# Kernel tuning notes

Hardware: AMD Instinct MI355X
Metric: run time of the kernel (lower is better)

The kernel has to match this reference:

```python
import jax, jax.numpy as jnp
import numpy as np


def _gcn_layer(feat, src, dst, W, b, n, act):
    # DGL GraphConv, norm='both': D_out^{-1/2} gather-sum D_in^{-1/2}, then XW+b
    e = src.shape[0]
    ones = jnp.ones((e,), dtype=feat.dtype)
    deg_out = jnp.clip(jax.ops.segment_sum(ones, src, num_segments=n), 1.0)
    deg_in = jnp.clip(jax.ops.segment_sum(ones, dst, num_segments=n), 1.0)
    h = feat * jax.lax.rsqrt(deg_out)[:, None]          # [n, d]
    agg = jax.ops.segment_sum(h[src], dst, num_segments=n)  # scatter-add over edges
    h = agg * jax.lax.rsqrt(deg_in)[:, None]
    h = h @ W + b
    if act:
        h = jax.nn.relu(h)
    return h


def setup_inputs() -> dict:
    key = jax.random.key(0)
    ks = jax.random.split(key, 12)
    n0, n1, n2 = 20000, 10000, 5000
    e0, e1, e2 = 640000, 320000, 160000
    in_dim, hid, ncls = 256, 128, 40
    s = 0.02
    return {
        "features": jax.random.normal(ks[0], (n0, in_dim), jnp.float32),
        "src0": jax.random.randint(ks[1], (e0,), 0, n0),
        "dst0": jax.random.randint(ks[2], (e0,), 0, n0),
        "src1": jax.random.randint(ks[3], (e1,), 0, n1),
        "dst1": jax.random.randint(ks[4], (e1,), 0, n1),
        "src2": jax.random.randint(ks[5], (e2,), 0, n2),
        "dst2": jax.random.randint(ks[6], (e2,), 0, n2),
        "P1": jax.random.normal(ks[7], (n0, n1), jnp.float32) * s,
        "P2": jax.random.normal(ks[8], (n1, n2), jnp.float32) * s,
        "W0": jax.random.normal(ks[9], (in_dim, hid), jnp.float32) * s,
        "b0": jnp.zeros((hid,), jnp.float32),
        "W1": jax.random.normal(ks[10], (hid, hid), jnp.float32) * s,
        "b1": jnp.zeros((hid,), jnp.float32),
        "W2": jax.random.normal(ks[11], (hid, ncls), jnp.float32) * s,
        "b2": jnp.zeros((ncls,), jnp.float32),
    }


def reference(features, src0, dst0, src1, dst1, src2, dst2, P1, P2,
              W0, b0, W1, b1, W2, b2):
    n0, n1, n2 = P1.shape[0], P1.shape[1], P2.shape[1]
    # layer 0 on finest graph (dropout is identity in eval mode)
    h = _gcn_layer(features, src0, dst0, W0, b0, n0, act=True)
    h = P1.T @ h                                  # project to level 1: [n1, hid]
    h = _gcn_layer(h, src1, dst1, W1, b1, n1, act=True)
    h = P2.T @ h                                  # project to level 2: [n2, hid]
    emb = h                                       # input to final layer
    h = _gcn_layer(h, src2, dst2, W2, b2, n2, act=False)
    return (h, emb)
```

## Files before the change

kernel.cpp:

```cpp
#include <hip/hip_runtime.h>
#include <stdint.h>

typedef __attribute__((ext_vector_type(8))) short s8v;
typedef __attribute__((ext_vector_type(4))) float f4v;

__device__ __forceinline__ unsigned short f2bf(float x){
  union { float f; uint32_t u; } v; v.f = x;
  uint32_t r = v.u + 0x7FFFu + ((v.u >> 16) & 1u);
  return (unsigned short)(r >> 16);
}
__device__ __forceinline__ float bf2f(unsigned short u){
  union { uint32_t u; float f; } v; v.u = ((uint32_t)u) << 16;
  return v.f;
}

__global__ __launch_bounds__(256) void k_cvt_feat(const float* __restrict__ in,
                                                  unsigned short* __restrict__ out, int n4){
  int i = blockIdx.x*256 + threadIdx.x;
  if (i >= n4) return;
  f4v v = ((const f4v*)in)[i];
  uint2 p;
  p.x = f2bf(v.x) | ((uint32_t)f2bf(v.y) << 16);
  p.y = f2bf(v.z) | ((uint32_t)f2bf(v.w) << 16);
  ((uint2*)out)[i] = p;
}

__global__ __launch_bounds__(256) void k_cvt_w(const float* __restrict__ W0, const float* __restrict__ W1,
                                               const float* __restrict__ W2,
                                               unsigned short* Wt0, unsigned short* Wt1, unsigned short* Wt2){
  int id = blockIdx.x*256 + threadIdx.x;
  if (id < 128*256){ int n = id >> 8, k = id & 255;
    Wt0[n*256 + (k ^ ((n&7)<<3))] = f2bf(W0[(size_t)k*128 + n]); return; }
  id -= 128*256;
  if (id < 128*128){ int n = id >> 7, k = id & 127;
    Wt1[n*128 + (k ^ ((n&7)<<3))] = f2bf(W1[(size_t)k*128 + n]); return; }
  id -= 128*128;
  if (id < 48*128){ int n = id >> 7, k = id & 127;
    Wt2[n*128 + (k ^ ((n&7)<<3))] = (n < 40) ? f2bf(W2[(size_t)k*40 + n]) : (unsigned short)0; return; }
}

__global__ __launch_bounds__(256) void k_count(
    const int* __restrict__ s0, const int* __restrict__ d0, int e0,
    const int* __restrict__ s1, const int* __restrict__ d1, int e1,
    const int* __restrict__ s2, const int* __restrict__ d2, int e2,
    int* ci0, int* co0, int* ci1, int* co1, int* ci2, int* co2,
    int* p0, int* p1, int* p2){
  int id = blockIdx.x*256 + threadIdx.x;
  if (id < e0){ p0[id] = atomicAdd(&ci0[d0[id]], 1); atomicAdd(&co0[s0[id]], 1); return; }
  id -= e0;
  if (id < e1){ p1[id] = atomicAdd(&ci1[d1[id]], 1); atomicAdd(&co1[s1[id]], 1); return; }
  id -= e1;
  if (id < e2){ p2[id] = atomicAdd(&ci2[d2[id]], 1); atomicAdd(&co2[s2[id]], 1); return; }
}

__global__ __launch_bounds__(1024) void k_scan3(const int* c0, int n0, int* o0,
                                                const int* c1, int n1, int* o1,
                                                const int* c2, int n2, int* o2){
  const int* c; int n; int* o;
  if (blockIdx.x == 0){ c = c0; n = n0; o = o0; }
  else if (blockIdx.x == 1){ c = c1; n = n1; o = o1; }
  else { c = c2; n = n2; o = o2; }
  __shared__ int part[1024];
  int t = threadIdx.x;
  int chunk = (n + 1023) / 1024;
  int beg = t*chunk, end = min(beg + chunk, n);
  int s = 0;
  for (int i = beg; i < end; i++) s += c[i];
  part[t] = s; __syncthreads();
  for (int d = 1; d < 1024; d <<= 1){
    int add = (t >= d) ? part[t-d] : 0;
    __syncthreads();
    part[t] += add;
    __syncthreads();
  }
  int prefix = (t > 0) ? part[t-1] : 0;
  for (int i = beg; i < end; i++){ o[i] = prefix; prefix += c[i]; }
  if (t == 1023) o[n] = part[1023];
}

__global__ __launch_bounds__(256) void k_place(
    const int* __restrict__ s0, const int* __restrict__ d0, int e0,
    const int* __restrict__ s1, const int* __restrict__ d1, int e1,
    const int* __restrict__ s2, const int* __restrict__ d2, int e2,
    const int* o0, const int* o1, const int* o2,
    const int* p0, const int* p1, const int* p2,
    int* r0, int* r1, int* r2){
  int id = blockIdx.x*256 + threadIdx.x;
  if (id < e0){ r0[o0[d0[id]] + p0[id]] = s0[id]; return; }
  id -= e0;
  if (id < e1){ r1[o1[d1[id]] + p1[id]] = s1[id]; return; }
  id -= e1;
  if (id < e2){ r2[o2[d2[id]] + p2[id]] = s2[id]; return; }
}

__global__ __launch_bounds__(256) void k_rsq(const int* ci0, const int* co0, int n0,
                                             const int* ci1, const int* co1, int n1,
                                             const int* ci2, const int* co2, int n2,
                                             float* ri0, float* ro0, float* ri1, float* ro1,
                                             float* ri2, float* ro2){
  int id = blockIdx.x*256 + threadIdx.x;
  if (id < n0){ ri0[id] = rsqrtf((float)max(ci0[id],1)); ro0[id] = rsqrtf((float)max(co0[id],1)); return; }
  id -= n0;
  if (id < n1){ ri1[id] = rsqrtf((float)max(ci1[id],1)); ro1[id] = rsqrtf((float)max(co1[id],1)); return; }
  id -= n1;
  if (id < n2){ ri2[id] = rsqrtf((float)max(ci2[id],1)); ro2[id] = rsqrtf((float)max(co2[id],1)); return; }
}

template<int D>
__global__ __launch_bounds__(256) void k_agg(const unsigned short* __restrict__ table,
                                             const int* __restrict__ srt, const int* __restrict__ off,
                                             const float* __restrict__ rsq_out, const float* __restrict__ rsq_in,
                                             unsigned short* __restrict__ outb, int n){
  constexpr int VW = D / 64;
  int wid = threadIdx.x >> 6, lane = threadIdx.x & 63;
  int node = blockIdx.x*4 + wid;
  if (node >= n) return;
  int eb = off[node], ee = off[node+1];
  float acc[VW];
  #pragma unroll
  for (int i = 0; i < VW; i++) acc[i] = 0.f;
  int c0 = lane * VW;
  int e = eb;
  int sNext = (e < ee) ? srt[e] : 0;
  while (e < ee){
    int s = sNext;
    e++;
    sNext = (e < ee) ? srt[e] : 0;
    float w = rsq_out[s];
    const unsigned short* row = table + (size_t)s*D + c0;
    if constexpr (VW == 4){
      ushort4 v = *(const ushort4*)row;
      acc[0] += w * bf2f(v.x); acc[1] += w * bf2f(v.y);
      acc[2] += w * bf2f(v.z); acc[3] += w * bf2f(v.w);
    } else {
      ushort2 v = *(const ushort2*)row;
      acc[0] += w * bf2f(v.x); acc[1] += w * bf2f(v.y);
    }
  }
  float ri = rsq_in[node];
  if constexpr (VW == 4){
    uint2 p;
    p.x = f2bf(acc[0]*ri) | ((uint32_t)f2bf(acc[1]*ri) << 16);
    p.y = f2bf(acc[2]*ri) | ((uint32_t)f2bf(acc[3]*ri) << 16);
    *(uint2*)(outb + (size_t)node*D + c0) = p;
  } else {
    uint32_t p = f2bf(acc[0]*ri) | ((uint32_t)f2bf(acc[1]*ri) << 16);
    *(uint32_t*)(outb + (size_t)node*D + c0) = p;
  }
}

template<int K, int NT, bool RELU>
__global__ __launch_bounds__(256) void k_gemm_nn(const unsigned short* __restrict__ A,
                                                 const unsigned short* __restrict__ Wt,
                                                 const float* __restrict__ bias,
                                                 unsigned short* __restrict__ outT,
                                                 float* __restrict__ outF,
                                                 int M, int ldOut, int Nv){
  __shared__ __align__(16) unsigned short lW[NT*16*K];
  for (int i = threadIdx.x; i < NT*16*K/8; i += 256)
    ((uint4*)lW)[i] = ((const uint4*)Wt)[i];
  __syncthreads();
  int lane = threadIdx.x & 63, w = threadIdx.x >> 6;
  int mb = blockIdx.x*64 + w*16;
  int row = mb + (lane & 15);
  int kg = lane >> 4;
  f4v acc[NT];
  #pragma unroll
  for (int nt = 0; nt < NT; nt++) acc[nt] = (f4v){0.f,0.f,0.f,0.f};
  for (int k0 = 0; k0 < K; k0 += 32){
    s8v a = {0,0,0,0,0,0,0,0};
    if (row < M) a = *(const s8v*)(A + (size_t)row*K + k0 + kg*8);
    #pragma unroll
    for (int nt = 0; nt < NT; nt++){
      int n = nt*16 + (lane & 15);
      s8v b = *(const s8v*)(lW + n*K + ((k0 + kg*8) ^ ((n&7)<<3)));
      acc[nt] = __builtin_amdgcn_mfma_f32_16x16x32_bf16(a, b, acc[nt], 0, 0, 0);
    }
  }
  int m4 = mb + kg*4;
  #pragma unroll
  for (int nt = 0; nt < NT; nt++){
    int n = nt*16 + (lane & 15);
    float bv = (n < Nv) ? bias[n] : 0.f;
    float v0 = acc[nt][0] + bv, v1 = acc[nt][1] + bv, v2 = acc[nt][2] + bv, v3 = acc[nt][3] + bv;
    if (RELU){ v0 = fmaxf(v0,0.f); v1 = fmaxf(v1,0.f); v2 = fmaxf(v2,0.f); v3 = fmaxf(v3,0.f); }
    if (outT){
      if (m4 >= M){ v0 = v1 = v2 = v3 = 0.f; }
      uint2 p;
      p.x = f2bf(v0) | ((uint32_t)f2bf(v1) << 16);
      p.y = f2bf(v2) | ((uint32_t)f2bf(v3) << 16);
      *(uint2*)(outT + (size_t)n*ldOut + (m4 ^ ((n&7)<<3))) = p;
    } else {
      float vv[4] = {v0, v1, v2, v3};
      #pragma unroll
      for (int r = 0; r < 4; r++){
        int m = m4 + r;
        if (m < M && n < Nv) outF[(size_t)m*Nv + n] = vv[r];
      }
    }
  }
}

__global__ __launch_bounds__(256) void k_tn(const float* __restrict__ P, int ldP, int M, int K,
                                            const unsigned short* __restrict__ Bsw, int ldB,
                                            float* __restrict__ part, int Mp,
                                            int KPtiles, int chunkTiles){
  __shared__ __align__(16) unsigned short lA[64*64];
  __shared__ __align__(16) unsigned short lB[128*64];
  int mb = blockIdx.x*64;
  int s  = blockIdx.y;
  int tbeg = s * chunkTiles;
  int tend = min(tbeg + chunkTiles, KPtiles);
  int tid = threadIdx.x, lane = tid & 63, w = tid >> 6;
  int wmBase = (w >> 1)*32, wnBase = (w & 1)*64;
  f4v acc[2][4];
  #pragma unroll
  for (int mt = 0; mt < 2; mt++)
    #pragma unroll
    for (int nt = 0; nt < 4; nt++) acc[mt][nt] = (f4v){0.f,0.f,0.f,0.f};

  for (int t = tbeg; t < tend; t++){
    int k0 = t*64;
    {
      int m2 = (tid & 31)*2;
      int kk = (tid >> 5)*2;
      int gm = mb + m2;
      #pragma unroll
      for (int p = 0; p < 4; p++){
        int kr = kk + p*16;
        int gk = k0 + kr;
        float2 r0 = {0.f,0.f}, r1 = {0.f,0.f};
        bool mok = (gm < M);
        if (mok && gk     < K) r0 = *(const float2*)(P + (size_t)gk*ldP + gm);
        if (mok && gk + 1 < K) r1 = *(const float2*)(P + (size_t)(gk+1)*ldP + gm);
        uint32_t w0 = f2bf(r0.x) | ((uint32_t)f2bf(r1.x) << 16);
        uint32_t w1 = f2bf(r0.y) | ((uint32_t)f2bf(r1.y) << 16);
        *(uint32_t*)(lA + m2*64     + (kr ^ ((m2&7)<<3)))     = w0;
        *(uint32_t*)(lA + (m2+1)*64 + (kr ^ (((m2+1)&7)<<3))) = w1;
      }
    }
    {
      int r  = tid >> 3;
      int cb = (tid & 7)*8;
      #pragma unroll
      for (int p = 0; p < 4; p++){
        int n = p*32 + r;
        uint4 v = *(const uint4*)(Bsw + (size_t)n*ldB + k0 + cb);
        *(uint4*)(lB + n*64 + cb) = v;
      }
    }
    __syncthreads();
    #pragma unroll
    for (int ks = 0; ks < 2; ks++){
      int kbase = ks*32 + (lane >> 4)*8;
      s8v a[2];
      #pragma unroll
      for (int mt = 0; mt < 2; mt++){
        int m = wmBase + mt*16 + (lane & 15);
        a[mt] = *(const s8v*)(lA + m*64 + (kbase ^ ((m&7)<<3)));
      }
      #pragma unroll
      for (int nt = 0; nt < 4; nt++){
        int n = wnBase + nt*16 + (lane & 15);
        s8v b = *(const s8v*)(lB + n*64 + (kbase ^ ((n&7)<<3)));
        #pragma unroll
        for (int mt = 0; mt < 2; mt++)
          acc[mt][nt] = __builtin_amdgcn_mfma_f32_16x16x32_bf16(a[mt], b, acc[mt][nt], 0, 0, 0);
      }
    }
    __syncthreads();
  }
  float* dst = part + (size_t)s*Mp*128;
  #pragma unroll
  for (int mt = 0; mt < 2; mt++){
    int m4 = mb + wmBase + mt*16 + (lane >> 4)*4;
    #pragma unroll
    for (int nt = 0; nt < 4; nt++){
      int n = wnBase + nt*16 + (lane & 15);
      #pragma unroll
      for (int r = 0; r < 4; r++)
        dst[(size_t)(m4 + r)*128 + n] = acc[mt][nt][r];
    }
  }
}

__global__ __launch_bounds__(256) void k_reduce(const float* __restrict__ part, int Mp, int S, int M,
                                                unsigned short* __restrict__ gb, float* __restrict__ embOut){
  int i = blockIdx.x*256 + threadIdx.x;
  int total = Mp*32;
  if (i >= total) return;
  f4v sum = (f4v){0.f,0.f,0.f,0.f};
  for (int p = 0; p < S; p++)
    sum += ((const f4v*)(part + (size_t)p*Mp*128))[i];
  int m = (i*4) >> 7;
  if (m < M){
    uint2 pk;
    pk.x = f2bf(sum.x) | ((uint32_t)f2bf(sum.y) << 16);
    pk.y = f2bf(sum.z) | ((uint32_t)f2bf(sum.w) << 16);
    ((uint2*)gb)[i] = pk;
    if (embOut) ((f4v*)embOut)[i] = sum;
  }
}

extern "C" void kernel_launch(void* const* d_in, const int* in_sizes, int n_in,
                              void* d_out, int out_size, void* d_ws, size_t ws_size,
                              hipStream_t stream){
  const float* features = (const float*)d_in[0];
  const int* src0 = (const int*)d_in[1];
  const int* dst0 = (const int*)d_in[2];
  const int* src1 = (const int*)d_in[3];
  const int* dst1 = (const int*)d_in[4];
  const int* src2 = (const int*)d_in[5];
  const int* dst2 = (const int*)d_in[6];
  const float* P1 = (const float*)d_in[7];
  const float* P2 = (const float*)d_in[8];
  const float* W0 = (const float*)d_in[9];
  const float* b0 = (const float*)d_in[10];
  const float* W1 = (const float*)d_in[11];
  const float* b1 = (const float*)d_in[12];
  const float* W2 = (const float*)d_in[13];
  const float* b2 = (const float*)d_in[14];
  float* out = (float*)d_out;

  const int IND = 256, HID = 128, NC = 40;
  const int n0 = in_sizes[0] / IND;
  const int e0 = in_sizes[1], e1 = in_sizes[3], e2 = in_sizes[5];
  const int n1 = (int)((size_t)in_sizes[7] / n0);
  const int n2 = (int)((size_t)in_sizes[8] / n1);

  const int g0   = (n0 + 63)/64;
  const int g1   = (n1 + 63)/64;
  const int g2   = (n2 + 63)/64;
  const int ld1  = g0*64;
  const int ld2  = g1*64;
  const int Mp1  = g1*64;
  const int Mp2  = g2*64;
  const int S1 = 6, S2 = 8;
  const int KPt1 = g0;
  const int KPt2 = g1;
  const int cT1 = (KPt1 + S1 - 1)/S1;
  const int cT2 = (KPt2 + S2 - 1)/S2;

  size_t o = 0;
  auto ALLOC = [&](size_t bytes)->size_t{ size_t r = o; o += (bytes + 255) & ~(size_t)255; return r; };
  size_t o_cnt = ALLOC((size_t)(2*n0 + 2*n1 + 2*n2)*4);
  size_t o_off = ALLOC((size_t)(n0 + n1 + n2 + 3)*4);
  size_t o_pos = ALLOC((size_t)(e0 + e1 + e2)*4);
  size_t o_srt = ALLOC((size_t)(e0 + e1 + e2)*4);
  size_t o_rsq = ALLOC((size_t)(2*n0 + 2*n1 + 2*n2)*4);
  size_t o_wt0 = ALLOC(128*256*2);
  size_t o_wt1 = ALLOC(128*128*2);
  size_t o_wt2 = ALLOC(48*128*2);
  size_t o_g1b = ALLOC((size_t)n1*128*2);
  size_t o_ag1 = ALLOC((size_t)n1*128*2);
  size_t o_h2t = ALLOC((size_t)128*ld2*2);
  size_t o_g2b = ALLOC((size_t)n2*128*2);
  size_t o_ag2 = ALLOC((size_t)n2*128*2);
  size_t o_h1t = ALLOC((size_t)128*ld1*2);
  size_t o_p1  = ALLOC((size_t)S1*Mp1*128*4);
  size_t featb_b = (size_t)n0*IND*2;
  size_t ovl_sz = featb_b*2;
  size_t p2_sz  = (size_t)S2*Mp2*128*4;
  if (p2_sz > ovl_sz) ovl_sz = p2_sz;
  size_t o_ovl = ALLOC(ovl_sz);
  if (ws_size < o) return;

  char* B = (char*)d_ws;
  int* ci0 = (int*)(B + o_cnt); int* co0 = ci0 + n0;
  int* ci1 = co0 + n0;          int* co1 = ci1 + n1;
  int* ci2 = co1 + n1;          int* co2 = ci2 + n2;
  int* off0 = (int*)(B + o_off); int* off1 = off0 + n0 + 1; int* off2 = off1 + n1 + 1;
  int* pos0 = (int*)(B + o_pos); int* pos1 = pos0 + e0; int* pos2 = pos1 + e1;
  int* srt0 = (int*)(B + o_srt); int* srt1 = srt0 + e0; int* srt2 = srt1 + e1;
  float* ri0 = (float*)(B + o_rsq); float* ro0 = ri0 + n0;
  float* ri1 = ro0 + n0; float* ro1 = ri1 + n1;
  float* ri2 = ro1 + n1; float* ro2 = ri2 + n2;
  unsigned short* wt0 = (unsigned short*)(B + o_wt0);
  unsigned short* wt1 = (unsigned short*)(B + o_wt1);
  unsigned short* wt2 = (unsigned short*)(B + o_wt2);
  unsigned short* g1b = (unsigned short*)(B + o_g1b);
  unsigned short* ag1 = (unsigned short*)(B + o_ag1);
  unsigned short* h2t = (unsigned short*)(B + o_h2t);
  unsigned short* g2b = (unsigned short*)(B + o_g2b);
  unsigned short* ag2 = (unsigned short*)(B + o_ag2);
  unsigned short* h1t = (unsigned short*)(B + o_h1t);
  float* part1 = (float*)(B + o_p1);
  unsigned short* featb = (unsigned short*)(B + o_ovl);
  unsigned short* ag0   = featb + featb_b/2;
  float* part2 = (float*)(B + o_ovl);

  float* emb = out + (size_t)n2*NC;

  hipMemsetAsync(B + o_cnt, 0, (size_t)(2*n0 + 2*n1 + 2*n2)*4, stream);
  k_cvt_w<<<216, 256, 0, stream>>>(W0, W1, W2, wt0, wt1, wt2);
  int n4f = n0*IND/4;
  k_cvt_feat<<<(n4f + 255)/256, 256, 0, stream>>>(features, featb, n4f);
  int eTot = e0 + e1 + e2;
  k_count<<<(eTot + 255)/256, 256, 0, stream>>>(src0, dst0, e0, src1, dst1, e1, src2, dst2, e2,
                                                ci0, co0, ci1, co1, ci2, co2, pos0, pos1, pos2);
  k_scan3<<<3, 1024, 0, stream>>>(ci0, n0, off0, ci1, n1, off1, ci2, n2, off2);
  k_place<<<(eTot + 255)/256, 256, 0, stream>>>(src0, dst0, e0, src1, dst1, e1, src2, dst2, e2,
                                                off0, off1, off2, pos0, pos1, pos2, srt0, srt1, srt2);
  k_rsq<<<((n0 + n1 + n2) + 255)/256, 256, 0, stream>>>(ci0, co0, n0, ci1, co1, n1, ci2, co2, n2,
                                                        ri0, ro0, ri1, ro1, ri2, ro2);
  k_agg<256><<<(n0 + 3)/4, 256, 0, stream>>>(featb, srt0, off0, ro0, ri0, ag0, n0);
  k_gemm_nn<256, 8, true><<<g0, 256, 0, stream>>>(ag0, wt0, b0, h1t, nullptr, n0, ld1, HID);
  {
    dim3 grid(g1, S1);
    k_tn<<<grid, 256, 0, stream>>>(P1, n1, n1, n0, h1t, ld1, part1, Mp1, KPt1, cT1);
  }
  k_reduce<<<(Mp1*32 + 255)/256, 256, 0, stream>>>(part1, Mp1, S1, n1, g1b, nullptr);
  k_agg<128><<<(n1 + 3)/4, 256, 0, stream>>>(g1b, srt1, off1, ro1, ri1, ag1, n1);
  k_gemm_nn<128, 8, true><<<g1, 256, 0, stream>>>(ag1, wt1, b1, h2t, nullptr, n1, ld2, HID);
  {
    dim3 grid(g2, S2);
    k_tn<<<grid, 256, 0, stream>>>(P2, n2, n2, n1, h2t, ld2, part2, Mp2, KPt2, cT2);
  }
  k_reduce<<<(Mp2*32 + 255)/256, 256, 0, stream>>>(part2, Mp2, S2, n2, g2b, emb);
  k_agg<128><<<(n2 + 3)/4, 256, 0, stream>>>(g2b, srt2, off2, ro2, ri2, ag2, n2);
  k_gemm_nn<128, 3, false><<<g2, 256, 0, stream>>>(ag2, wt2, b2, nullptr, out, n2, 0, NC);
}
```

Before: 610.3 us.

## Reorder GCN layers to transform before aggregating and double-buffer projection GEMM

```diff
diff --git a/kernel.cpp b/kernel.cpp
--- a/kernel.cpp
+++ b/kernel.cpp
@@ -14,15 +14,9 @@
   return v.f;
 }
 
-__global__ __launch_bounds__(256) void k_cvt_feat(const float* __restrict__ in,
-                                                  unsigned short* __restrict__ out, int n4){
-  int i = blockIdx.x*256 + threadIdx.x;
-  if (i >= n4) return;
-  f4v v = ((const f4v*)in)[i];
-  uint2 p;
-  p.x = f2bf(v.x) | ((uint32_t)f2bf(v.y) << 16);
-  p.y = f2bf(v.z) | ((uint32_t)f2bf(v.w) << 16);
-  ((uint2*)out)[i] = p;
+__device__ __forceinline__ void gload_lds16(const void* g, void* l){
+  __builtin_amdgcn_global_load_lds((const __attribute__((address_space(1))) void*)g,
+                                   (__attribute__((address_space(3))) void*)l, 16, 0, 0);
 }
 
 __global__ __launch_bounds__(256) void k_cvt_w(const float* __restrict__ W0, const float* __restrict__ W1,
@@ -106,56 +100,12 @@
   if (id < n2){ ri2[id] = rsqrtf((float)max(ci2[id],1)); ro2[id] = rsqrtf((float)max(co2[id],1)); return; }
 }
 
-template<int D>
-__global__ __launch_bounds__(256) void k_agg(const unsigned short* __restrict__ table,
-                                             const int* __restrict__ srt, const int* __restrict__ off,
-                                             const float* __restrict__ rsq_out, const float* __restrict__ rsq_in,
-                                             unsigned short* __restrict__ outb, int n){
-  constexpr int VW = D / 64;
-  int wid = threadIdx.x >> 6, lane = threadIdx.x & 63;
-  int node = blockIdx.x*4 + wid;
-  if (node >= n) return;
-  int eb = off[node], ee = off[node+1];
-  float acc[VW];
-  #pragma unroll
-  for (int i = 0; i < VW; i++) acc[i] = 0.f;
-  int c0 = lane * VW;
-  int e = eb;
-  int sNext = (e < ee) ? srt[e] : 0;
-  while (e < ee){
-    int s = sNext;
-    e++;
-    sNext = (e < ee) ? srt[e] : 0;
-    float w = rsq_out[s];
-    const unsigned short* row = table + (size_t)s*D + c0;
-    if constexpr (VW == 4){
-      ushort4 v = *(const ushort4*)row;
-      acc[0] += w * bf2f(v.x); acc[1] += w * bf2f(v.y);
-      acc[2] += w * bf2f(v.z); acc[3] += w * bf2f(v.w);
-    } else {
-      ushort2 v = *(const ushort2*)row;
-      acc[0] += w * bf2f(v.x); acc[1] += w * bf2f(v.y);
-    }
-  }
-  float ri = rsq_in[node];
-  if constexpr (VW == 4){
-    uint2 p;
-    p.x = f2bf(acc[0]*ri) | ((uint32_t)f2bf(acc[1]*ri) << 16);
-    p.y = f2bf(acc[2]*ri) | ((uint32_t)f2bf(acc[3]*ri) << 16);
-    *(uint2*)(outb + (size_t)node*D + c0) = p;
-  } else {
-    uint32_t p = f2bf(acc[0]*ri) | ((uint32_t)f2bf(acc[1]*ri) << 16);
-    *(uint32_t*)(outb + (size_t)node*D + c0) = p;
-  }
-}
-
-template<int K, int NT, bool RELU>
-__global__ __launch_bounds__(256) void k_gemm_nn(const unsigned short* __restrict__ A,
+template<int K, int NT, bool AF32>
+__global__ __launch_bounds__(256) void k_gemm_rs(const void* __restrict__ Av,
                                                  const unsigned short* __restrict__ Wt,
-                                                 const float* __restrict__ bias,
-                                                 unsigned short* __restrict__ outT,
-                                                 float* __restrict__ outF,
-                                                 int M, int ldOut, int Nv){
+                                                 const float* __restrict__ scale,
+                                                 unsigned short* __restrict__ Y, int M){
+  constexpr int LDY = NT*16;
   __shared__ __align__(16) unsigned short lW[NT*16*K];
   for (int i = threadIdx.x; i < NT*16*K/8; i += 256)
     ((uint4*)lW)[i] = ((const uint4*)Wt)[i];
@@ -169,7 +119,17 @@
   for (int nt = 0; nt < NT; nt++) acc[nt] = (f4v){0.f,0.f,0.f,0.f};
   for (int k0 = 0; k0 < K; k0 += 32){
     s8v a = {0,0,0,0,0,0,0,0};
-    if (row < M) a = *(const s8v*)(A + (size_t)row*K + k0 + kg*8);
+    if (row < M){
+      if (AF32){
+        const float* ap = (const float*)Av + (size_t)row*K + k0 + kg*8;
+        f4v f0 = *(const f4v*)ap;
+        f4v f1 = *(const f4v*)(ap + 4);
+        a[0]=(short)f2bf(f0.x); a[1]=(short)f2bf(f0.y); a[2]=(short)f2bf(f0.z); a[3]=(short)f2bf(f0.w);
+        a[4]=(short)f2bf(f1.x); a[5]=(short)f2bf(f1.y); a[6]=(short)f2bf(f1.z); a[7]=(short)f2bf(f1.w);
+      } else {
+        a = *(const s8v*)((const unsigned short*)Av + (size_t)row*K + k0 + kg*8);
+      }
+    }
     #pragma unroll
     for (int nt = 0; nt < NT; nt++){
       int n = nt*16 + (lane & 15);
@@ -181,105 +141,184 @@
   #pragma unroll
   for (int nt = 0; nt < NT; nt++){
     int n = nt*16 + (lane & 15);
-    float bv = (n < Nv) ? bias[n] : 0.f;
-    float v0 = acc[nt][0] + bv, v1 = acc[nt][1] + bv, v2 = acc[nt][2] + bv, v3 = acc[nt][3] + bv;
-    if (RELU){ v0 = fmaxf(v0,0.f); v1 = fmaxf(v1,0.f); v2 = fmaxf(v2,0.f); v3 = fmaxf(v3,0.f); }
-    if (outT){
-      if (m4 >= M){ v0 = v1 = v2 = v3 = 0.f; }
-      uint2 p;
-      p.x = f2bf(v0) | ((uint32_t)f2bf(v1) << 16);
-      p.y = f2bf(v2) | ((uint32_t)f2bf(v3) << 16);
-      *(uint2*)(outT + (size_t)n*ldOut + (m4 ^ ((n&7)<<3))) = p;
-    } else {
-      float vv[4] = {v0, v1, v2, v3};
-      #pragma unroll
-      for (int r = 0; r < 4; r++){
-        int m = m4 + r;
-        if (m < M && n < Nv) outF[(size_t)m*Nv + n] = vv[r];
+    #pragma unroll
+    for (int r = 0; r < 4; r++){
+      int m = m4 + r;
+      if (m < M) Y[(size_t)m*LDY + n] = f2bf(acc[nt][r] * scale[m]);
+    }
+  }
+}
+
+__global__ __launch_bounds__(512) void k_aggT(const unsigned short* __restrict__ Y,
+                                              const int* __restrict__ srt, const int* __restrict__ off,
+                                              const float* __restrict__ ri, const float* __restrict__ bias,
+                                              unsigned short* __restrict__ hT, int ld, int n){
+  __shared__ unsigned short ls[128*40];
+  int tid = threadIdx.x, lane = tid & 63, wid = tid >> 6;
+  for (int i = tid; i < 128*40/2; i += 512) ((uint32_t*)ls)[i] = 0;
+  __syncthreads();
+  int base = blockIdx.x*32;
+  int c0 = lane*2;
+  for (int i = 0; i < 4; i++){
+    int node = base + wid*4 + i;
+    if (node < n){
+      int eb = off[node], ee = off[node+1];
+      float a0 = 0.f, a1 = 0.f;
+      int e = eb;
+      int sn = (e < ee) ? srt[e] : 0;
+      while (e < ee){
+        int sc = sn; e++;
+        sn = (e < ee) ? srt[e] : 0;
+        uint32_t v = *(const uint32_t*)(Y + (size_t)sc*128 + c0);
+        a0 += bf2f((unsigned short)v);
+        a1 += bf2f((unsigned short)(v >> 16));
       }
-    }
+      float r = ri[node];
+      float h0 = fmaxf(a0*r + bias[c0],   0.f);
+      float h1 = fmaxf(a1*r + bias[c0+1], 0.f);
+      int nl = node - base;
+      ls[c0*40 + nl]     = f2bf(h0);
+      ls[(c0+1)*40 + nl] = f2bf(h1);
+    }
+  }
+  __syncthreads();
+  int d = tid >> 2, c = tid & 3;
+  uint4 v = *(const uint4*)(ls + d*40 + c*8);
+  int m8 = base + c*8;
+  *(uint4*)(hT + (size_t)d*ld + (m8 ^ ((d&7)<<3))) = v;
+}
+
+__global__ __launch_bounds__(256) void k_agg2(const unsigned short* __restrict__ Z,
+                                              const int* __restrict__ srt, const int* __restrict__ off,
+                                              const float* __restrict__ ri, const float* __restrict__ bias,
+                                              float* __restrict__ out, int n){
+  int lane = threadIdx.x & 63, wid = threadIdx.x >> 6;
+  int node = blockIdx.x*4 + wid;
+  if (node >= n) return;
+  int eb = off[node], ee = off[node+1];
+  int c0 = lane*2;
+  bool act = lane < 24;
+  float a0 = 0.f, a1 = 0.f;
+  int e = eb;
+  int sn = (e < ee) ? srt[e] : 0;
+  while (e < ee){
+    int sc = sn; e++;
+    sn = (e < ee) ? srt[e] : 0;
+    if (act){
+      uint32_t v = *(const uint32_t*)(Z + (size_t)sc*48 + c0);
+      a0 += bf2f((unsigned short)v);
+      a1 += bf2f((unsigned short)(v >> 16));
+    }
+  }
+  if (c0 < 40){
+    float r = ri[node];
+    float2 o2 = { a0*r + bias[c0], a1*r + bias[c0+1] };
+    *(float2*)(out + (size_t)node*40 + c0) = o2;
   }
 }
 
 __global__ __launch_bounds__(256) void k_tn(const float* __restrict__ P, int ldP, int M, int K,
-                                            const unsigned short* __restrict__ Bsw, int ldB,
+                                            const unsigned short* __restrict__ hT, int ld,
                                             float* __restrict__ part, int Mp,
                                             int KPtiles, int chunkTiles){
-  __shared__ __align__(16) unsigned short lA[64*64];
-  __shared__ __align__(16) unsigned short lB[128*64];
-  int mb = blockIdx.x*64;
+  __shared__ __align__(16) unsigned short lA[128*64];
+  __shared__ __align__(16) unsigned short lB[2][128*64];
+  int tid = threadIdx.x, lane = tid & 63, w = tid >> 6;
+  int mb = blockIdx.x*128;
   int s  = blockIdx.y;
-  int tbeg = s * chunkTiles;
-  int tend = min(tbeg + chunkTiles, KPtiles);
-  int tid = threadIdx.x, lane = tid & 63, w = tid >> 6;
-  int wmBase = (w >> 1)*32, wnBase = (w & 1)*64;
-  f4v acc[2][4];
+  int tbeg = s*chunkTiles, tend = min(tbeg + chunkTiles, KPtiles);
+  int m2 = (tid & 63)*2;
+  int kb = (tid >> 6)*2;
+  int gm = mb + m2;
+  bool mok = gm < M;
+  float2 ra[8], rb[8];
+
+  auto LOADA = [&](int t){
+    int k0 = t*64;
+    #pragma unroll
+    for (int p = 0; p < 8; p++){
+      int gk = k0 + kb + p*8;
+      float2 z = {0.f, 0.f};
+      ra[p] = z; rb[p] = z;
+      if (mok && gk     < K) ra[p] = *(const float2*)(P + (size_t)gk*ldP + gm);
+      if (mok && gk + 1 < K) rb[p] = *(const float2*)(P + (size_t)(gk+1)*ldP + gm);
+    }
+  };
+  auto WRITEA = [&](){
+    #pragma unroll
+    for (int p = 0; p < 8; p++){
+      int kr = kb + p*8;
+      uint32_t w0 = f2bf(ra[p].x) | ((uint32_t)f2bf(rb[p].x) << 16);
+      uint32_t w1 = f2bf(ra[p].y) | ((uint32_t)f2bf(rb[p].y) << 16);
+      *(uint32_t*)(lA + m2*64     + (kr ^ ((m2&7)<<3)))     = w0;
+      *(uint32_t*)(lA + (m2+1)*64 + (kr ^ (((m2+1)&7)<<3))) = w1;
+    }
+  };
+  auto ISSUEB = [&](int t, int buf){
+    size_t k0b = (size_t)t*64*2;
+    char* lbase = (char*)&lB[buf][0];
+    #pragma unroll
+    for (int it = 0; it < 4; it++){
+      int chunkByte = (it*4 + w)*1024;
+      int myByte = chunkByte + lane*16;
+      int nrow = myByte >> 7;
+      int koff = myByte & 127;
+      const char* src = (const char*)hT + (size_t)nrow*ld*2 + k0b + koff;
+      gload_lds16(src, lbase + chunkByte);
+    }
+  };
+
+  int wmBase = (w & 1)*64, wnBase = (w >> 1)*64;
+  f4v acc[4][4];
   #pragma unroll
-  for (int mt = 0; mt < 2; mt++)
+  for (int mt = 0; mt < 4; mt++)
     #pragma unroll
     for (int nt = 0; nt < 4; nt++) acc[mt][nt] = (f4v){0.f,0.f,0.f,0.f};
 
-  for (int t = tbeg; t < tend; t++){
-    int k0 = t*64;
-    {
-      int m2 = (tid & 31)*2;
-      int kk = (tid >> 5)*2;
-      int gm = mb + m2;
-      #pragma unroll
-      for (int p = 0; p < 4; p++){
-        int kr = kk + p*16;
-        int gk = k0 + kr;
-        float2 r0 = {0.f,0.f}, r1 = {0.f,0.f};
-        bool mok = (gm < M);
-        if (mok && gk     < K) r0 = *(const float2*)(P + (size_t)gk*ldP + gm);
-        if (mok && gk + 1 < K) r1 = *(const float2*)(P + (size_t)(gk+1)*ldP + gm);
-        uint32_t w0 = f2bf(r0.x) | ((uint32_t)f2bf(r1.x) << 16);
-        uint32_t w1 = f2bf(r0.y) | ((uint32_t)f2bf(r1.y) << 16);
-        *(uint32_t*)(lA + m2*64     + (kr ^ ((m2&7)<<3)))     = w0;
-        *(uint32_t*)(lA + (m2+1)*64 + (kr ^ (((m2+1)&7)<<3))) = w1;
-      }
-    }
-    {
-      int r  = tid >> 3;
-      int cb = (tid & 7)*8;
-      #pragma unroll
-      for (int p = 0; p < 4; p++){
-        int n = p*32 + r;
-        uint4 v = *(const uint4*)(Bsw + (size_t)n*ldB + k0 + cb);
-        *(uint4*)(lB + n*64 + cb) = v;
-      }
-    }
-    __syncthreads();
+  auto COMPUTE = [&](int buf){
     #pragma unroll
     for (int ks = 0; ks < 2; ks++){
       int kbase = ks*32 + (lane >> 4)*8;
-      s8v a[2];
+      s8v af[4];
       #pragma unroll
-      for (int mt = 0; mt < 2; mt++){
+      for (int mt = 0; mt < 4; mt++){
         int m = wmBase + mt*16 + (lane & 15);
-        a[mt] = *(const s8v*)(lA + m*64 + (kbase ^ ((m&7)<<3)));
+        af[mt] = *(const s8v*)(lA + m*64 + (kbase ^ ((m&7)<<3)));
       }
       #pragma unroll
       for (int nt = 0; nt < 4; nt++){
-        int n = wnBase + nt*16 + (lane & 15);
-        s8v b = *(const s8v*)(lB + n*64 + (kbase ^ ((n&7)<<3)));
+        int nn = wnBase + nt*16 + (lane & 15);
+        s8v bf = *(const s8v*)(&lB[buf][0] + nn*64 + (kbase ^ ((nn&7)<<3)));
         #pragma unroll
-        for (int mt = 0; mt < 2; mt++)
-          acc[mt][nt] = __builtin_amdgcn_mfma_f32_16x16x32_bf16(a[mt], b, acc[mt][nt], 0, 0, 0);
+        for (int mt = 0; mt < 4; mt++)
+          acc[mt][nt] = __builtin_amdgcn_mfma_f32_16x16x32_bf16(af[mt], bf, acc[mt][nt], 0, 0, 0);
       }
     }
+  };
+
+  LOADA(tbeg);
+  ISSUEB(tbeg, 0);
+  WRITEA();
+  __syncthreads();
+  for (int t = tbeg; t < tend; t++){
+    int cur = (t - tbeg) & 1;
+    bool more = (t + 1 < tend);
+    if (more){ ISSUEB(t + 1, cur ^ 1); LOADA(t + 1); }
+    COMPUTE(cur);
+    __syncthreads();
+    if (more) WRITEA();
     __syncthreads();
   }
   float* dst = part + (size_t)s*Mp*128;
   #pragma unroll
-  for (int mt = 0; mt < 2; mt++){
+  for (int mt = 0; mt < 4; mt++){
     int m4 = mb + wmBase + mt*16 + (lane >> 4)*4;
     #pragma unroll
     for (int nt = 0; nt < 4; nt++){
-      int n = wnBase + nt*16 + (lane & 15);
+      int nn = wnBase + nt*16 + (lane & 15);
       #pragma unroll
       for (int r = 0; r < 4; r++)
-        dst[(size_t)(m4 + r)*128 + n] = acc[mt][nt][r];
+        dst[(size_t)(m4 + r)*128 + nn] = acc[mt][nt][r];
     }
   }
 }
@@ -292,7 +331,7 @@
   f4v sum = (f4v){0.f,0.f,0.f,0.f};
   for (int p = 0; p < S; p++)
     sum += ((const f4v*)(part + (size_t)p*Mp*128))[i];
-  int m = (i*4) >> 7;
+  int m = i >> 5;
   if (m < M){
     uint2 pk;
     pk.x = f2bf(sum.x) | ((uint32_t)f2bf(sum.y) << 16);
@@ -322,22 +361,19 @@
   const float* b2 = (const float*)d_in[14];
   float* out = (float*)d_out;
 
-  const int IND = 256, HID = 128, NC = 40;
+  const int IND = 256, NC = 40;
   const int n0 = in_sizes[0] / IND;
   const int e0 = in_sizes[1], e1 = in_sizes[3], e2 = in_sizes[5];
   const int n1 = (int)((size_t)in_sizes[7] / n0);
   const int n2 = (int)((size_t)in_sizes[8] / n1);
 
-  const int g0   = (n0 + 63)/64;
-  const int g1   = (n1 + 63)/64;
-  const int g2   = (n2 + 63)/64;
-  const int ld1  = g0*64;
-  const int ld2  = g1*64;
-  const int Mp1  = g1*64;
-  const int Mp2  = g2*64;
-  const int S1 = 6, S2 = 8;
-  const int KPt1 = g0;
-  const int KPt2 = g1;
+  const int KPt1 = (n0 + 63)/64;
+  const int KPt2 = (n1 + 63)/64;
+  const int ld1  = KPt1*64;
+  const int ld2  = KPt2*64;
+  const int Mp1  = ((n1 + 127)/128)*128;
+  const int Mp2  = ((n2 + 127)/128)*128;
+  const int S1 = 8, S2 = 12;
   const int cT1 = (KPt1 + S1 - 1)/S1;
   const int cT2 = (KPt2 + S2 - 1)/S2;
 
@@ -351,18 +387,15 @@
   size_t o_wt0 = ALLOC(128*256*2);
   size_t o_wt1 = ALLOC(128*128*2);
   size_t o_wt2 = ALLOC(48*128*2);
-  size_t o_g1b = ALLOC((size_t)n1*128*2);
-  size_t o_ag1 = ALLOC((size_t)n1*128*2);
-  size_t o_h2t = ALLOC((size_t)128*ld2*2);
-  size_t o_g2b = ALLOC((size_t)n2*128*2);
-  size_t o_ag2 = ALLOC((size_t)n2*128*2);
+  size_t o_y0  = ALLOC((size_t)n0*128*2);
   size_t o_h1t = ALLOC((size_t)128*ld1*2);
   size_t o_p1  = ALLOC((size_t)S1*Mp1*128*4);
-  size_t featb_b = (size_t)n0*IND*2;
-  size_t ovl_sz = featb_b*2;
-  size_t p2_sz  = (size_t)S2*Mp2*128*4;
-  if (p2_sz > ovl_sz) ovl_sz = p2_sz;
-  size_t o_ovl = ALLOC(ovl_sz);
+  size_t o_g1  = ALLOC((size_t)n1*128*2);
+  size_t o_y1  = ALLOC((size_t)n1*128*2);
+  size_t o_h2t = ALLOC((size_t)128*ld2*2);
+  size_t o_p2  = ALLOC((size_t)S2*Mp2*128*4);
+  size_t o_emb = ALLOC((size_t)n2*128*2);
+  size_t o_z2  = ALLOC((size_t)n2*48*2);
   if (ws_size < o) return;
 
   char* B = (char*)d_ws;
@@ -378,23 +411,22 @@
   unsigned short* wt0 = (unsigned short*)(B + o_wt0);
   unsigned short* wt1 = (unsigned short*)(B + o_wt1);
   unsigned short* wt2 = (unsigned short*)(B + o_wt2);
-  unsigned short* g1b = (unsigned short*)(B + o_g1b);
-  unsigned short* ag1 = (unsigned short*)(B + o_ag1);
-  unsigned short* h2t = (unsigned short*)(B + o_h2t);
-  unsigned short* g2b = (unsigned short*)(B + o_g2b);
-  unsigned short* ag2 = (unsigned short*)(B + o_ag2);
+  unsigned short* Y0  = (unsigned short*)(B + o_y0);
   unsigned short* h1t = (unsigned short*)(B + o_h1t);
   float* part1 = (float*)(B + o_p1);
-  unsigned short* featb = (unsigned short*)(B + o_ovl);
-  unsigned short* ag0   = featb + featb_b/2;
-  float* part2 = (float*)(B + o_ovl);
+  unsigned short* g1  = (unsigned short*)(B + o_g1);
+  unsigned short* Y1  = (unsigned short*)(B + o_y1);
+  unsigned short* h2t = (unsigned short*)(B + o_h2t);
+  float* part2 = (float*)(B + o_p2);
+  unsigned short* embb = (unsigned short*)(B + o_emb);
+  unsigned short* Z2  = (unsigned short*)(B + o_z2);
 
   float* emb = out + (size_t)n2*NC;
 
   hipMemsetAsync(B + o_cnt, 0, (size_t)(2*n0 + 2*n1 + 2*n2)*4, stream);
+  hipMemsetAsync(h1t, 0, (size_t)128*ld1*2, stream);
+  hipMemsetAsync(h2t, 0, (size_t)128*ld2*2, stream);
   k_cvt_w<<<216, 256, 0, stream>>>(W0, W1, W2, wt0, wt1, wt2);
-  int n4f = n0*IND/4;
-  k_cvt_feat<<<(n4f + 255)/256, 256, 0, stream>>>(features, featb, n4f);
   int eTot = e0 + e1 + e2;
   k_count<<<(eTot + 255)/256, 256, 0, stream>>>(src0, dst0, e0, src1, dst1, e1, src2, dst2, e2,
                                                 ci0, co0, ci1, co1, ci2, co2, pos0, pos1, pos2);
@@ -403,20 +435,20 @@
                                                 off0, off1, off2, pos0, pos1, pos2, srt0, srt1, srt2);
   k_rsq<<<((n0 + n1 + n2) + 255)/256, 256, 0, stream>>>(ci0, co0, n0, ci1, co1, n1, ci2, co2, n2,
                                                         ri0, ro0, ri1, ro1, ri2, ro2);
-  k_agg<256><<<(n0 + 3)/4, 256, 0, stream>>>(featb, srt0, off0, ro0, ri0, ag0, n0);
-  k_gemm_nn<256, 8, true><<<g0, 256, 0, stream>>>(ag0, wt0, b0, h1t, nullptr, n0, ld1, HID);
+  k_gemm_rs<256, 8, true><<<(n0 + 63)/64, 256, 0, stream>>>(features, wt0, ro0, Y0, n0);
+  k_aggT<<<(n0 + 31)/32, 512, 0, stream>>>(Y0, srt0, off0, ri0, b0, h1t, ld1, n0);
   {
-    dim3 grid(g1, S1);
+    dim3 grid(Mp1/128, S1);
     k_tn<<<grid, 256, 0, stream>>>(P1, n1, n1, n0, h1t, ld1, part1, Mp1, KPt1, cT1);
   }
-  k_reduce<<<(Mp1*32 + 255)/256, 256, 0, stream>>>(part1, Mp1, S1, n1, g1b, nullptr);
-  k_agg<128><<<(n1 + 3)/4, 256, 0, stream>>>(g1b, srt1, off1, ro1, ri1, ag1, n1);
-  k_gemm_nn<128, 8, true><<<g1, 256, 0, stream>>>(ag1, wt1, b1, h2t, nullptr, n1, ld2, HID);
+  k_reduce<<<(Mp1*32 + 255)/256, 256, 0, stream>>>(part1, Mp1, S1, n1, g1, nullptr);
+  k_gemm_rs<128, 8, false><<<(n1 + 63)/64, 256, 0, stream>>>(g1, wt1, ro1, Y1, n1);
+  k_aggT<<<(n1 + 31)/32, 512, 0, stream>>>(Y1, srt1, off1, ri1, b1, h2t, ld2, n1);
   {
-    dim3 grid(g2, S2);
+    dim3 grid(Mp2/128, S2);
     k_tn<<<grid, 256, 0, stream>>>(P2, n2, n2, n1, h2t, ld2, part2, Mp2, KPt2, cT2);
   }
-  k_reduce<<<(Mp2*32 + 255)/256, 256, 0, stream>>>(part2, Mp2, S2, n2, g2b, emb);
-  k_agg<128><<<(n2 + 3)/4, 256, 0, stream>>>(g2b, srt2, off2, ro2, ri2, ag2, n2);
-  k_gemm_nn<128, 3, false><<<g2, 256, 0, stream>>>(ag2, wt2, b2, nullptr, out, n2, 0, NC);
-}
+  k_reduce<<<(Mp2*32 + 255)/256, 256, 0, stream>>>(part2, Mp2, S2, n2, embb, emb);
+  k_gemm_rs<128, 3, false><<<(n2 + 63)/64, 256, 0, stream>>>(embb, wt2, ro2, Z2, n2);
+  k_agg2<<<(n2 + 3)/4, 256, 0, stream>>>(Z2, srt2, off2, ri2, b2, out, n2);
+}
```

Result: no change. 610.0 us (-0.0%).
